# Kernel optimization log

Measured on AMD Instinct MI355X. Metric: run time of the kernel, lower is better.

The kernel has to match this reference:

```python
import jax, jax.numpy as jnp
import numpy as np

H = 128          # input hidden dim
HID = 128        # expert hidden width
OUT = 128        # out_channels
NR = 8           # n_routed
NS = 2           # n_shared
RDIM = 16        # router feature dim


def setup_inputs() -> dict:
    key = jax.random.key(0)
    ks = jax.random.split(key, 11)
    s = 0.05
    x = jax.random.normal(ks[0], (2, 32, 32, 32, H), dtype=jnp.float32)
    # router params
    Wr1 = jax.random.normal(ks[1], (H, RDIM), dtype=jnp.float32) * s
    br1 = jnp.zeros((RDIM,), dtype=jnp.float32)
    Wr2 = jax.random.normal(ks[2], (RDIM, NR), dtype=jnp.float32) * s
    br2 = jnp.zeros((NR,), dtype=jnp.float32)
    # routed expert params, stacked on leading expert axis
    We1 = jax.random.normal(ks[3], (NR, H, HID), dtype=jnp.float32) * s
    be1 = jnp.zeros((NR, HID), dtype=jnp.float32)
    We2 = jax.random.normal(ks[4], (NR, HID, OUT), dtype=jnp.float32) * s
    be2 = jnp.zeros((NR, OUT), dtype=jnp.float32)
    # shared expert params
    Ws1 = jax.random.normal(ks[5], (NS, H, HID), dtype=jnp.float32) * s
    bs1 = jnp.zeros((NS, HID), dtype=jnp.float32)
    Ws2 = jax.random.normal(ks[6], (NS, HID, OUT), dtype=jnp.float32) * s
    bs2 = jnp.zeros((NS, OUT), dtype=jnp.float32)
    return dict(x=x, Wr1=Wr1, br1=br1, Wr2=Wr2, br2=br2,
                We1=We1, be1=be1, We2=We2, be2=be2,
                Ws1=Ws1, bs1=bs1, Ws2=Ws2, bs2=bs2)


def reference(x, Wr1, br1, Wr2, br2, We1, be1, We2, be2, Ws1, bs1, Ws2, bs2):
    # router: Dense(16) -> relu -> Dense(n_routed) -> softmax
    rf = jax.nn.relu(jnp.einsum('...h,hr->...r', x, Wr1) + br1)
    logits = jnp.einsum('...r,re->...e', rf, Wr2) + br2
    gate = jax.nn.softmax(logits, axis=-1)                      # [..., NR]
    threshold = 1.0 / NR
    mask = (gate > threshold).astype(gate.dtype)
    mg = gate * mask
    mg = mg / (jnp.sum(mg, axis=-1, keepdims=True) + 1e-8)
    # routed experts (batched over expert axis e): Dense -> gelu(tanh) -> Dense
    hr = jax.nn.gelu(jnp.einsum('...h,ehd->...ed', x, We1) + be1)   # [..., NR, HID]
    ro = jnp.einsum('...ed,edo->...eo', hr, We2) + be2              # [..., NR, OUT]
    routed_agg = jnp.einsum('...eo,...e->...o', ro, mg)
    # shared experts summed
    hs = jax.nn.gelu(jnp.einsum('...h,ehd->...ed', x, Ws1) + bs1)   # [..., NS, HID]
    so = jnp.einsum('...ed,edo->...eo', hs, Ws2) + bs2              # [..., NS, OUT]
    shared_agg = jnp.sum(so, axis=-2)
    return routed_agg + shared_agg
```

## Files before the change

kernel.cpp:

```cpp
#include <hip/hip_runtime.h>
#include <hip/hip_bf16.h>

typedef __bf16 bf16x8 __attribute__((ext_vector_type(8)));
typedef float  f32x16 __attribute__((ext_vector_type(16)));
typedef float  f32x4  __attribute__((ext_vector_type(4)));
typedef float  f32x2  __attribute__((ext_vector_type(2)));

static __device__ __forceinline__ f32x16 mfma32(bf16x8 a, bf16x8 b, f32x16 c) {
    return __builtin_amdgcn_mfma_f32_32x32x16_bf16(a, b, c, 0, 0, 0);
}

#define GELU_C1 2.30220820f
#define GELU_C2 0.10294324f

__global__ __launch_bounds__(256) void pack_kernel(
    const float* __restrict__ We1, const float* __restrict__ be1,
    const float* __restrict__ Ws1, const float* __restrict__ bs1,
    const float* __restrict__ We2, const float* __restrict__ Ws2,
    const float* __restrict__ Wr1, const float* __restrict__ br1,
    const float* __restrict__ Wr2, const float* __restrict__ br2,
    __bf16* __restrict__ w1p, __bf16* __restrict__ w2p,
    double* __restrict__ wr1d, double* __restrict__ br1d,
    double* __restrict__ wr2d, double* __restrict__ br2d)
{
    int tid = blockIdx.x * 256 + threadIdx.x;
    if (tid < 23040) {
        int l  = tid & 63;
        int ks = (tid >> 6) % 9;
        int nt = (tid / 576) & 3;
        int e  = tid / 2304;
        const float* src = (e < 8) ? (We1 + e * 16384) : (Ws1 + (e - 8) * 16384);
        const float* bia = (e < 8) ? (be1 + e * 128)   : (bs1 + (e - 8) * 128);
        int n = nt * 32 + (l & 31);
        int kb = ks * 16 + (l >> 5) * 8;
        bf16x8 v;
        #pragma unroll
        for (int j = 0; j < 8; ++j) {
            int k = kb + j;
            float f = (k < 128) ? src[k * 128 + n] : ((k == 128) ? bia[n] : 0.f);
            v[j] = (__bf16)f;
        }
        *(bf16x8*)(w1p + (size_t)tid * 8) = v;
    } else if (tid < 43520) {
        int t2 = tid - 23040;
        int l  = t2 & 63;
        int ks = (t2 >> 6) & 7;
        int ot = (t2 / 512) & 3;
        int e  = t2 / 2048;
        const float* src = (e < 8) ? (We2 + e * 16384) : (Ws2 + (e - 8) * 16384);
        int o  = ot * 32 + (l & 31);
        int lh = l >> 5;
        bf16x8 v;
        #pragma unroll
        for (int j = 0; j < 8; ++j) {
            int hid = 16 * ks + 8 * (j >> 2) + 4 * lh + (j & 3);
            v[j] = (__bf16)src[hid * 128 + o];
        }
        *(bf16x8*)(w2p + (size_t)t2 * 8) = v;
    } else if (tid < 45568) {
        int i = tid - 43520;
        wr1d[i] = (double)Wr1[i];
    } else if (tid < 45696) {
        int i = tid - 45568;
        wr2d[i] = (double)Wr2[i];
    } else if (tid < 45712) {
        int i = tid - 45696;
        br1d[i] = (double)br1[i];
    } else if (tid < 45720) {
        int i = tid - 45712;
        br2d[i] = (double)br2[i];
    }
}

__global__ __launch_bounds__(256, 2) void moe_main_kernel(
    const float* __restrict__ x,
    const double* __restrict__ wr1d, const double* __restrict__ br1d,
    const double* __restrict__ wr2d, const double* __restrict__ br2d,
    const __bf16* __restrict__ w1p, const __bf16* __restrict__ w2p,
    const float* __restrict__ be2, const float* __restrict__ bs2,
    float* __restrict__ out)
{
    __shared__ __align__(16) char lds[61952];
    float*  xs  = (float*)lds;
    __bf16* Xp  = (__bf16*)(lds + 33280);
    double* rfs = (double*)(lds + 51712);
    float*  mgs = (float*)(lds + 59904);
    float*  Red = (float*)lds;

    const int t    = threadIdx.x;
    const int lane = t & 63;
    const int wave = t >> 6;
    const int l31  = lane & 31;
    const int lh   = lane >> 5;
    const int mt   = wave >> 1;
    const int h    = wave & 1;
    const int tok0 = blockIdx.x * 64;

    #pragma unroll
    for (int i = 0; i < 4; ++i) {
        int g = i * 256 + t;
        int m = g >> 4;
        int c = g & 15;
        const f32x4* sp = (const f32x4*)(x + (size_t)(tok0 + m) * 128 + c * 8);
        f32x4 va = sp[0], vb = sp[1];
        float* xd = xs + m * 130 + c * 8;
        f32x2 s0, s1, s2, s3;
        s0[0]=va[0]; s0[1]=va[1]; s1[0]=va[2]; s1[1]=va[3];
        s2[0]=vb[0]; s2[1]=vb[1]; s3[0]=vb[2]; s3[1]=vb[3];
        *(f32x2*)(xd)     = s0; *(f32x2*)(xd + 2) = s1;
        *(f32x2*)(xd + 4) = s2; *(f32x2*)(xd + 6) = s3;
        bf16x8 v;
        v[0]=(__bf16)va[0]; v[1]=(__bf16)va[1]; v[2]=(__bf16)va[2]; v[3]=(__bf16)va[3];
        v[4]=(__bf16)vb[0]; v[5]=(__bf16)vb[1]; v[6]=(__bf16)vb[2]; v[7]=(__bf16)vb[3];
        *(bf16x8*)&Xp[(((m >> 5) * 9 + (c >> 1)) * 64 + (c & 1) * 32 + (m & 31)) * 8] = v;
    }
    if (t < 128) {
        int mtx = t >> 6, l = t & 63;
        bf16x8 v;
        #pragma unroll
        for (int j = 0; j < 8; ++j) v[j] = (__bf16)0.f;
        if (l < 32) v[0] = (__bf16)1.0f;
        *(bf16x8*)&Xp[((mtx * 9 + 8) * 64 + l) * 8] = v;
    }
    __syncthreads();

    {
        const int tok = t & 63;
        const int rq  = (t >> 6) * 4;
        const int rqs = __builtin_amdgcn_readfirstlane(rq);
        double rf4[4];
        #pragma unroll
        for (int j = 0; j < 4; ++j) rf4[j] = br1d[rqs + j];
        const float* xr = xs + tok * 130;
        #pragma unroll 4
        for (int c = 0; c < 64; ++c) {
            f32x2 xv2 = *(const f32x2*)(xr + c * 2);
            #pragma unroll
            for (int q = 0; q < 2; ++q) {
                double xv = (double)xv2[q];
                int k = c * 2 + q;
                #pragma unroll
                for (int j = 0; j < 4; ++j)
                    rf4[j] = fma(xv, wr1d[k * 16 + rqs + j], rf4[j]);
            }
        }
        #pragma unroll
        for (int j = 0; j < 4; ++j)
            rfs[tok * 16 + rq + j] = rf4[j] > 0.0 ? rf4[j] : 0.0;
    }
    __syncthreads();

    if (t < 64) {
        double lg[8];
        #pragma unroll
        for (int j = 0; j < 8; ++j) lg[j] = br2d[j];
        #pragma unroll
        for (int r = 0; r < 16; ++r) {
            double rv = rfs[t * 16 + r];
            #pragma unroll
            for (int j = 0; j < 8; ++j)
                lg[j] = fma(rv, wr2d[r * 8 + j], lg[j]);
        }
        double mx = lg[0];
        #pragma unroll
        for (int j = 1; j < 8; ++j) mx = lg[j] > mx ? lg[j] : mx;
        double ex[8]; double s = 0.0;
        #pragma unroll
        for (int j = 0; j < 8; ++j) { ex[j] = exp(lg[j] - mx); s += ex[j]; }
        double ms = 0.0;
        bool mk[8];
        #pragma unroll
        for (int j = 0; j < 8; ++j) {
            mk[j] = (8.0 * ex[j] > s);
            ms += mk[j] ? ex[j] : 0.0;
        }
        double inv = 1.0 / (ms + s * 1e-8);
        #pragma unroll
        for (int j = 0; j < 8; ++j)
            mgs[t * 8 + j] = mk[j] ? (float)(ex[j] * inv) : 0.f;
    }
    __syncthreads();

    const float* mgr = mgs + (32 * mt + l31) * 8;
    f32x4 ga4 = *(const f32x4*)mgr;
    f32x4 gb4 = *(const f32x4*)(mgr + 4);
    float gte[8] = {ga4[0], ga4[1], ga4[2], ga4[3], gb4[0], gb4[1], gb4[2], gb4[3]};

    f32x16 acc[4];
    #pragma unroll
    for (int ot = 0; ot < 4; ++ot)
        #pragma unroll
        for (int i = 0; i < 16; ++i) acc[ot][i] = 0.f;

    const bf16x8* w1v = (const bf16x8*)w1p;
    const bf16x8* w2v = (const bf16x8*)w2p;

    bf16x8 wbuf[2][9];
    {
        const bf16x8* p = w1v + ((size_t)(2 * h) * 9) * 64 + lane;
        #pragma unroll
        for (int ks = 0; ks < 9; ++ks) wbuf[0][ks] = p[ks * 64];
    }

    #pragma unroll 1
    for (int e = 0; e < 10; ++e) {
        const float gv = (e < 8) ? gte[e] : 1.0f;
        #pragma unroll
        for (int n2 = 0; n2 < 2; ++n2) {
            const bf16x8* wBp = w2v + ((size_t)(e * 4) * 8 + 4 * h + 2 * n2) * 64 + lane;
            bf16x8 wBc[8];
            #pragma unroll
            for (int ot = 0; ot < 4; ++ot)
                #pragma unroll
                for (int b = 0; b < 2; ++b)
                    wBc[ot * 2 + b] = wBp[(ot * 8 + b) * 64];

            f32x16 a1;
            #pragma unroll
            for (int i = 0; i < 16; ++i) a1[i] = 0.f;
            #pragma unroll
            for (int ks = 0; ks < 9; ++ks) {
                bf16x8 xb = *(const bf16x8*)&Xp[((mt * 9 + ks) * 64 + lane) * 8];
                a1 = mfma32(wbuf[n2][ks], xb, a1);
            }

            {
                int en  = (n2 == 0) ? e : (e < 9 ? e + 1 : 9);
                int ntn = (n2 == 0) ? (2 * h + 1) : (2 * h);
                const bf16x8* p = w1v + ((size_t)(en * 4 + ntn) * 9) * 64 + lane;
                #pragma unroll
                for (int ks = 0; ks < 9; ++ks) wbuf[n2 ^ 1][ks] = p[ks * 64];
            }

            #pragma unroll
            for (int b = 0; b < 2; ++b) {
                bf16x8 fr;
                #pragma unroll
                for (int jp = 0; jp < 4; ++jp) {
                    f32x2 hh; hh[0] = a1[8 * b + 2 * jp]; hh[1] = a1[8 * b + 2 * jp + 1];
                    f32x2 tt = hh * hh;
                    f32x2 pp;
                    pp[0] = fmaf(tt[0], -GELU_C2, -GELU_C1);
                    pp[1] = fmaf(tt[1], -GELU_C2, -GELU_C1);
                    f32x2 mm = hh * pp;
                    float e0 = __builtin_amdgcn_exp2f(mm[0]);
                    float e1 = __builtin_amdgcn_exp2f(mm[1]);
                    float q0 = __builtin_amdgcn_rcpf(1.f + e0);
                    float q1 = __builtin_amdgcn_rcpf(1.f + e1);
                    f32x2 gg; gg[0] = hh[0] * q0 * gv; gg[1] = hh[1] * q1 * gv;
                    fr[2 * jp]     = (__bf16)gg[0];
                    fr[2 * jp + 1] = (__bf16)gg[1];
                }
                acc[0] = mfma32(fr, wBc[0 * 2 + b], acc[0]);
                acc[1] = mfma32(fr, wBc[1 * 2 + b], acc[1]);
                acc[2] = mfma32(fr, wBc[2 * 2 + b], acc[2]);
                acc[3] = mfma32(fr, wBc[3 * 2 + b], acc[3]);
            }
        }
    }

    __syncthreads();
    if (h == 1) {
        #pragma unroll
        for (int ot = 0; ot < 4; ++ot)
            #pragma unroll
            for (int r = 0; r < 16; ++r)
                Red[((mt * 4 + ot) * 16 + r) * 64 + lane] = acc[ot][r];
    }
    __syncthreads();
    if (h == 0) {
        float be2c[4][8], bsc[4];
        #pragma unroll
        for (int ot = 0; ot < 4; ++ot) {
            int o = 32 * ot + l31;
            bsc[ot] = bs2[o] + bs2[128 + o];
            #pragma unroll
            for (int ee = 0; ee < 8; ++ee) be2c[ot][ee] = be2[ee * 128 + o];
        }
        const float* mgb = mgs + (32 * mt) * 8;
        #pragma unroll
        for (int r = 0; r < 16; ++r) {
            int mrow = (r & 3) + 8 * (r >> 2) + 4 * lh;
            f32x4 g0 = *(const f32x4*)&mgb[mrow * 8];
            f32x4 g1 = *(const f32x4*)&mgb[mrow * 8 + 4];
            size_t orow = (size_t)(tok0 + 32 * mt + mrow) * 128;
            #pragma unroll
            for (int ot = 0; ot < 4; ++ot) {
                float b = bsc[ot];
                #pragma unroll
                for (int ee = 0; ee < 4; ++ee) b = fmaf(g0[ee], be2c[ot][ee], b);
                #pragma unroll
                for (int ee = 0; ee < 4; ++ee) b = fmaf(g1[ee], be2c[ot][4 + ee], b);
                float v = acc[ot][r] + Red[((mt * 4 + ot) * 16 + r) * 64 + lane] + b;
                out[orow + 32 * ot + l31] = v;
            }
        }
    }
}

extern "C" void kernel_launch(void* const* d_in, const int* in_sizes, int n_in,
                              void* d_out, int out_size, void* d_ws, size_t ws_size,
                              hipStream_t stream)
{
    const float* x   = (const float*)d_in[0];
    const float* Wr1 = (const float*)d_in[1];
    const float* br1 = (const float*)d_in[2];
    const float* Wr2 = (const float*)d_in[3];
    const float* br2 = (const float*)d_in[4];
    const float* We1 = (const float*)d_in[5];
    const float* be1 = (const float*)d_in[6];
    const float* We2 = (const float*)d_in[7];
    const float* be2 = (const float*)d_in[8];
    const float* Ws1 = (const float*)d_in[9];
    const float* bs1 = (const float*)d_in[10];
    const float* Ws2 = (const float*)d_in[11];
    const float* bs2 = (const float*)d_in[12];

    __bf16* w1p  = (__bf16*)d_ws;
    __bf16* w2p  = (__bf16*)((char*)d_ws + 368640);
    double* wr1d = (double*)((char*)d_ws + 696320);
    double* wr2d = (double*)((char*)d_ws + 712704);
    double* br1d = (double*)((char*)d_ws + 713728);
    double* br2d = (double*)((char*)d_ws + 713856);

    pack_kernel<<<179, 256, 0, stream>>>(We1, be1, Ws1, bs1, We2, Ws2,
                                         Wr1, br1, Wr2, br2,
                                         w1p, w2p, wr1d, br1d, wr2d, br2d);
    moe_main_kernel<<<1024, 256, 0, stream>>>(x, wr1d, br1d, wr2d, br2d,
                                              w1p, w2p, be2, bs2, (float*)d_out);
}
```

Before: 176.5 us.

## Raise occupancy to 3 blocks/CU by shrinking LDS and dropping W1 prefetch buffer

Shrinks the per-block LDS footprint by overlapping the fp32 x staging buffer and the router feature buffer, and changes the row pitch to 131. Launch bounds now ask for 3 blocks per CU. The double-buffered register prefetch of W1 fragments is replaced with a load just before use, which frees registers for the higher occupancy. The trade-off is that W1 global load latency is no longer hidden behind the previous MFMA chain and now has to be covered by the extra resident waves. Because the buffers now alias, an extra barrier is needed before the router features are written.

```diff
diff --git a/kernel.cpp b/kernel.cpp
--- a/kernel.cpp
+++ b/kernel.cpp
@@ -72,7 +72,7 @@
     }
 }
 
-__global__ __launch_bounds__(256, 2) void moe_main_kernel(
+__global__ __launch_bounds__(256, 3) void moe_main_kernel(
     const float* __restrict__ x,
     const double* __restrict__ wr1d, const double* __restrict__ br1d,
     const double* __restrict__ wr2d, const double* __restrict__ br2d,
@@ -80,11 +80,11 @@
     const float* __restrict__ be2, const float* __restrict__ bs2,
     float* __restrict__ out)
 {
-    __shared__ __align__(16) char lds[61952];
-    float*  xs  = (float*)lds;
-    __bf16* Xp  = (__bf16*)(lds + 33280);
-    double* rfs = (double*)(lds + 51712);
-    float*  mgs = (float*)(lds + 59904);
+    __shared__ __align__(16) char lds[51968];
+    __bf16* Xp  = (__bf16*)lds;
+    float*  xs  = (float*)(lds + 18432);
+    double* rfs = (double*)(lds + 18432);
+    float*  mgs = (float*)(lds + 49920);
     float*  Red = (float*)lds;
 
     const int t    = threadIdx.x;
@@ -103,12 +103,9 @@
         int c = g & 15;
         const f32x4* sp = (const f32x4*)(x + (size_t)(tok0 + m) * 128 + c * 8);
         f32x4 va = sp[0], vb = sp[1];
-        float* xd = xs + m * 130 + c * 8;
-        f32x2 s0, s1, s2, s3;
-        s0[0]=va[0]; s0[1]=va[1]; s1[0]=va[2]; s1[1]=va[3];
-        s2[0]=vb[0]; s2[1]=vb[1]; s3[0]=vb[2]; s3[1]=vb[3];
-        *(f32x2*)(xd)     = s0; *(f32x2*)(xd + 2) = s1;
-        *(f32x2*)(xd + 4) = s2; *(f32x2*)(xd + 6) = s3;
+        float* xd = xs + m * 131 + c * 8;
+        xd[0] = va[0]; xd[1] = va[1]; xd[2] = va[2]; xd[3] = va[3];
+        xd[4] = vb[0]; xd[5] = vb[1]; xd[6] = vb[2]; xd[7] = vb[3];
         bf16x8 v;
         v[0]=(__bf16)va[0]; v[1]=(__bf16)va[1]; v[2]=(__bf16)va[2]; v[3]=(__bf16)va[3];
         v[4]=(__bf16)vb[0]; v[5]=(__bf16)vb[1]; v[6]=(__bf16)vb[2]; v[7]=(__bf16)vb[3];
@@ -124,29 +121,30 @@
     }
     __syncthreads();
 
+    double rf4[4];
+    {
+        const int tok = t & 63;
+        const int rqs = __builtin_amdgcn_readfirstlane((t >> 6) * 4);
+        #pragma unroll
+        for (int j = 0; j < 4; ++j) rf4[j] = br1d[rqs + j];
+        const float* xr = xs + tok * 131;
+        #pragma unroll 8
+        for (int k = 0; k < 128; ++k) {
+            double xv = (double)xr[k];
+            #pragma unroll
+            for (int j = 0; j < 4; ++j)
+                rf4[j] = fma(xv, wr1d[k * 16 + rqs + j], rf4[j]);
+        }
+        #pragma unroll
+        for (int j = 0; j < 4; ++j) rf4[j] = rf4[j] > 0.0 ? rf4[j] : 0.0;
+    }
+    __syncthreads();
+
     {
         const int tok = t & 63;
         const int rq  = (t >> 6) * 4;
-        const int rqs = __builtin_amdgcn_readfirstlane(rq);
-        double rf4[4];
-        #pragma unroll
-        for (int j = 0; j < 4; ++j) rf4[j] = br1d[rqs + j];
-        const float* xr = xs + tok * 130;
-        #pragma unroll 4
-        for (int c = 0; c < 64; ++c) {
-            f32x2 xv2 = *(const f32x2*)(xr + c * 2);
-            #pragma unroll
-            for (int q = 0; q < 2; ++q) {
-                double xv = (double)xv2[q];
-                int k = c * 2 + q;
-                #pragma unroll
-                for (int j = 0; j < 4; ++j)
-                    rf4[j] = fma(xv, wr1d[k * 16 + rqs + j], rf4[j]);
-            }
-        }
-        #pragma unroll
-        for (int j = 0; j < 4; ++j)
-            rfs[tok * 16 + rq + j] = rf4[j] > 0.0 ? rf4[j] : 0.0;
+        #pragma unroll
+        for (int j = 0; j < 4; ++j) rfs[tok * 16 + rq + j] = rf4[j];
     }
     __syncthreads();
 
@@ -195,18 +193,16 @@
     const bf16x8* w1v = (const bf16x8*)w1p;
     const bf16x8* w2v = (const bf16x8*)w2p;
 
-    bf16x8 wbuf[2][9];
-    {
-        const bf16x8* p = w1v + ((size_t)(2 * h) * 9) * 64 + lane;
-        #pragma unroll
-        for (int ks = 0; ks < 9; ++ks) wbuf[0][ks] = p[ks * 64];
-    }
-
     #pragma unroll 1
     for (int e = 0; e < 10; ++e) {
         const float gv = (e < 8) ? gte[e] : 1.0f;
         #pragma unroll
         for (int n2 = 0; n2 < 2; ++n2) {
+            const bf16x8* wap = w1v + ((size_t)(e * 4 + 2 * h + n2) * 9) * 64 + lane;
+            bf16x8 wb[9];
+            #pragma unroll
+            for (int ks = 0; ks < 9; ++ks) wb[ks] = wap[ks * 64];
+
             const bf16x8* wBp = w2v + ((size_t)(e * 4) * 8 + 4 * h + 2 * n2) * 64 + lane;
             bf16x8 wBc[8];
             #pragma unroll
@@ -221,15 +217,7 @@
             #pragma unroll
             for (int ks = 0; ks < 9; ++ks) {
                 bf16x8 xb = *(const bf16x8*)&Xp[((mt * 9 + ks) * 64 + lane) * 8];
-                a1 = mfma32(wbuf[n2][ks], xb, a1);
-            }
-
-            {
-                int en  = (n2 == 0) ? e : (e < 9 ? e + 1 : 9);
-                int ntn = (n2 == 0) ? (2 * h + 1) : (2 * h);
-                const bf16x8* p = w1v + ((size_t)(en * 4 + ntn) * 9) * 64 + lane;
-                #pragma unroll
-                for (int ks = 0; ks < 9; ++ks) wbuf[n2 ^ 1][ks] = p[ks * 64];
+                a1 = mfma32(wb[ks], xb, a1);
             }
 
             #pragma unroll
```

Measured after the change: 214.9 us. 1.22x slower.
